# Optimization experiments

Hardware: AMD Instinct MI355X
Metric: run time of the kernel (lower is better)

The kernel has to match this reference:

```python
import jax, jax.numpy as jnp
import numpy as np

BSZ, SEQ, D, NHEAD, NLAYER, DFF, NQ = 4, 48, 256, 2, 2, 2048, 512
LN_EPS = 1e-5
NEG = jnp.float32(-1e30)


def _layernorm(x, w, b):
    m = jnp.mean(x, axis=-1, keepdims=True)
    v = jnp.mean((x - m) ** 2, axis=-1, keepdims=True)
    return (x - m) / jnp.sqrt(v + LN_EPS) * w + b


def _span_max(x):
    # Cumulative span max: span[b,s,e] = max(x[b,s:e+1]) for e>=s, else 0.
    B, S, H = x.shape
    padded = jnp.concatenate([x, jnp.full((B, S, H), NEG, x.dtype)], axis=1)  # [B,2S,H]

    def step(tmp, i):
        shifted = jax.lax.dynamic_slice(padded, (0, i, 0), (B, S, H))  # x shifted left by i, padded with -inf
        tmp = jnp.maximum(tmp, shifted)  # tmp[b,s] = max(x[b,s:s+i+1])
        return tmp, tmp

    _, ys = jax.lax.scan(step, jnp.full((B, S, H), NEG, x.dtype), jnp.arange(S))
    # ys: [width, B, start, H]; span[b,s,e] = ys[e-s, b, s]
    si = jnp.arange(S)[:, None]
    ei = jnp.arange(S)[None, :]
    w = jnp.clip(ei - si, 0, S - 1)
    span = ys[w, :, jnp.broadcast_to(si, (S, S))]  # [S_start, S_end, B, H]
    span = jnp.where((ei >= si)[:, :, None, None], span, 0.0)
    return span.transpose(2, 0, 1, 3)  # [B,S,S,H]


def _mha(x, wi, bi, wo, bo, kpm):
    # x: [B,T,D]; kpm: [B,T] bool, True = masked key
    B, T, Dm = x.shape
    hd = Dm // NHEAD
    qkv = x @ wi.T + bi
    q, k, v = jnp.split(qkv, 3, axis=-1)
    rs = lambda a: a.reshape(B, T, NHEAD, hd).transpose(0, 2, 1, 3)
    q, k, v = rs(q), rs(k), rs(v)
    scores = jnp.einsum('bhqd,bhkd->bhqk', q, k) * (1.0 / np.sqrt(hd))
    scores = jnp.where(kpm[:, None, None, :], -1e9, scores)
    p = jax.nn.softmax(scores, axis=-1)
    o = jnp.einsum('bhqk,bhkd->bhqd', p, v).transpose(0, 2, 1, 3).reshape(B, T, Dm)
    return o @ wo.T + bo


def _encoder(x, kpm, iw, ib, ow, ob, l1w, l1b, l2w, l2b, f1w, f1b, f2w, f2b, fw, fb):
    # Post-norm torch TransformerEncoder (eval mode, relu, no dropout)
    for l in range(NLAYER):
        a = _mha(x, iw[l], ib[l], ow[l], ob[l], kpm)
        x = _layernorm(x + a, l1w[l], l1b[l])
        f = jax.nn.relu(x @ f1w[l].T + f1b[l]) @ f2w[l].T + f2b[l]
        x = _layernorm(x + f, l2w[l], l2b[l])
    return _layernorm(x, fw, fb)


def _forward(enc, iw, ib, ow, ob, l1w, l1b, l2w, l2b, f1w, f1b, f2w, f2b, fw, fb, s1, e1, qb, s2, e2):
    span = _span_max(enc)  # [B,S,S,D]
    idx = jnp.arange(SEQ)
    kpm2d = idx[None, :] < idx[:, None]  # [start,end]: True where end < start
    kpm = jnp.broadcast_to(kpm2d.reshape(1, SEQ * SEQ), (BSZ, SEQ * SEQ))
    out = _encoder(span.reshape(BSZ, SEQ * SEQ, D), kpm, iw, ib, ow, ob, l1w, l1b, l2w, l2b, f1w, f1b, f2w, f2b, fw, fb)
    out = out.reshape(BSZ, SEQ, SEQ, D)
    res1 = out[qb, s1, e1]
    res2 = out[qb, s2, e2]
    return res1, res2


def setup_inputs() -> dict:
    key = jax.random.key(0)
    ks = jax.random.split(key, 16)
    sc = 0.02
    enc = jax.random.normal(ks[0], (BSZ, SEQ, D), jnp.float32)
    inp = {
        'encoded_input': enc,
        'in_proj_w': jax.random.normal(ks[1], (NLAYER, 3 * D, D), jnp.float32) * sc,
        'in_proj_b': jnp.zeros((NLAYER, 3 * D), jnp.float32),
        'out_proj_w': jax.random.normal(ks[2], (NLAYER, D, D), jnp.float32) * sc,
        'out_proj_b': jnp.zeros((NLAYER, D), jnp.float32),
        'ln1_w': jnp.ones((NLAYER, D), jnp.float32),
        'ln1_b': jnp.zeros((NLAYER, D), jnp.float32),
        'ln2_w': jnp.ones((NLAYER, D), jnp.float32),
        'ln2_b': jnp.zeros((NLAYER, D), jnp.float32),
        'ff1_w': jax.random.normal(ks[3], (NLAYER, DFF, D), jnp.float32) * sc,
        'ff1_b': jnp.zeros((NLAYER, DFF), jnp.float32),
        'ff2_w': jax.random.normal(ks[4], (NLAYER, D, DFF), jnp.float32) * sc,
        'ff2_b': jnp.zeros((NLAYER, D), jnp.float32),
        'fln_w': jnp.ones((D,), jnp.float32),
        'fln_b': jnp.zeros((D,), jnp.float32),
    }
    s1 = jax.random.randint(ks[5], (NQ,), 0, SEQ)
    e1 = jnp.minimum(s1 + jax.random.randint(ks[6], (NQ,), 0, SEQ), SEQ - 1)
    s2 = jax.random.randint(ks[7], (NQ,), 0, SEQ)
    e2 = jnp.minimum(s2 + jax.random.randint(ks[8], (NQ,), 0, SEQ), SEQ - 1)
    inp['start_ids_1'] = s1
    inp['end_ids_1'] = e1
    inp['query_batch_idx'] = jax.random.randint(ks[9], (NQ,), 0, BSZ)
    inp['start_ids_2'] = s2
    inp['end_ids_2'] = e2
    return inp


def reference(encoded_input, in_proj_w, in_proj_b, out_proj_w, out_proj_b, ln1_w, ln1_b, ln2_w, ln2_b, ff1_w, ff1_b, ff2_w, ff2_b, fln_w, fln_b, start_ids_1, end_ids_1, query_batch_idx, start_ids_2, end_ids_2):
    return _forward(encoded_input, in_proj_w, in_proj_b, out_proj_w, out_proj_b, ln1_w, ln1_b, ln2_w, ln2_b, ff1_w, ff1_b, ff2_w, ff2_b, fln_w, fln_b, start_ids_1, end_ids_1, query_batch_idx, start_ids_2, end_ids_2)
```

## Files before the change

kernel.cpp:

```cpp
#include <hip/hip_runtime.h>
#include <hip/hip_bf16.h>

#define BSZ 4
#define SEQ 48
#define DMODEL 256
#define NHEAD 2
#define HD 128
#define NLAYERS 2
#define DFF_C 2048
#define NQ_C 512
#define NV 1176
#define NTOT (BSZ * NV)
#define NVP 1216
#define KSPLIT 5
#define SCALE 0.088388347648318447f

typedef unsigned short u16;
typedef __attribute__((ext_vector_type(8))) short bf16x8;
typedef __attribute__((ext_vector_type(4))) float f32x4;

__device__ inline u16 f2b(float f) {
    __hip_bfloat16 h = __float2bfloat16(f);
    return *reinterpret_cast<u16*>(&h);
}
__device__ inline void storeval(float* p, float v) { *p = v; }
__device__ inline void storeval(u16* p, float v) { *p = f2b(v); }

__global__ __launch_bounds__(256) void castspan_kernel(
    const float* __restrict__ iw, const float* __restrict__ ow,
    const float* __restrict__ f1w, const float* __restrict__ f2w,
    u16* __restrict__ iwb, u16* __restrict__ owb,
    u16* __restrict__ f1wb, u16* __restrict__ f2wb,
    const float* __restrict__ enc, float* __restrict__ X,
    u16* __restrict__ Xb) {
    int bid = blockIdx.x;
    if (bid < 2560) {
        int i = bid * 256 + threadIdx.x;
        const float* src;
        u16* dst;
        int off;
        if (i < 98304)       { src = iw;  dst = iwb;  off = i; }
        else if (i < 131072) { src = ow;  dst = owb;  off = i - 98304; }
        else if (i < 393216) { src = f1w; dst = f1wb; off = i - 131072; }
        else                 { src = f2w; dst = f2wb; off = i - 393216; }
        float4 v = *(const float4*)(src + (size_t)off * 4);
        *(ushort4*)(dst + (size_t)off * 4) =
            make_ushort4(f2b(v.x), f2b(v.y), f2b(v.z), f2b(v.w));
    } else {
        int sb = bid - 2560;
        int i = sb % SEQ, b = sb / SEQ, h = threadIdx.x;
        int tb = i * SEQ - (i * (i - 1)) / 2 - i;
        float run = -1e30f;
        for (int j = i; j < SEQ; ++j) {
            run = fmaxf(run, enc[((size_t)b * SEQ + j) * DMODEL + h]);
            size_t idx = ((size_t)b * NV + tb + j) * DMODEL + h;
            X[idx] = run;
            Xb[idx] = f2b(run);
        }
    }
}

template <typename OutT, bool RELU, bool ATOMIC, int BK>
__global__ __launch_bounds__(256) void mm_kernel(
    const u16* __restrict__ A, const u16* __restrict__ W,
    const float* __restrict__ bias, const float* __restrict__ Res,
    OutT* __restrict__ C, int N, int K, int lda, int ldw, int ldc,
    float alpha, int WV, int KC) {
    __shared__ u16 As[64][BK + 8];
    __shared__ u16 Ws[64][BK + 8];
    const float4 fz = make_float4(0.f, 0.f, 0.f, 0.f);
    int ks = blockIdx.z;
    int kb = ks * KC, ke = min(K, kb + KC);
    int p0 = blockIdx.x * 64, n0 = blockIdx.y * 64;
    int tid = threadIdx.x, lane = tid & 63, w = tid >> 6;
    int col_l = lane & 15, quad = lane >> 4;
    f32x4 acc[4] = {};
    for (int k0 = kb; k0 < ke; k0 += BK) {
        int r = tid >> 2, seg = (tid & 3) * (BK / 4);
        {
            int gn = n0 + r;
            const u16* ap = A + (size_t)gn * lda + k0 + seg;
#pragma unroll
            for (int j = 0; j < BK / 32; ++j) {
                float4 av = fz;
                if (gn < N) av = *(const float4*)(ap + j * 8);
                *(float4*)&As[r][seg + j * 8] = av;
            }
        }
        {
            int gp = p0 + r;
            const u16* wp = W + (size_t)gp * ldw + k0 + seg;
#pragma unroll
            for (int j = 0; j < BK / 32; ++j) {
                float4 wv = fz;
                if (gp < WV) wv = *(const float4*)(wp + j * 8);
                *(float4*)&Ws[r][seg + j * 8] = wv;
            }
        }
        __syncthreads();
        bf16x8 a[BK / 32];
#pragma unroll
        for (int kf = 0; kf < BK / 32; ++kf)
            a[kf] = *(const bf16x8*)&As[w * 16 + col_l][kf * 32 + quad * 8];
#pragma unroll
        for (int c = 0; c < 4; ++c) {
#pragma unroll
            for (int kf = 0; kf < BK / 32; ++kf) {
                bf16x8 b = *(const bf16x8*)&Ws[c * 16 + col_l][kf * 32 + quad * 8];
                acc[c] = __builtin_amdgcn_mfma_f32_16x16x32_bf16(a[kf], b, acc[c], 0, 0, 0);
            }
        }
        __syncthreads();
    }
#pragma unroll
    for (int c = 0; c < 4; ++c) {
        int col = p0 + c * 16 + col_l;
        float bv = bias ? bias[col] : 0.f;
#pragma unroll
        for (int reg = 0; reg < 4; ++reg) {
            int row = n0 + w * 16 + quad * 4 + reg;
            if (row < N) {
                float v = acc[c][reg] * alpha + bv;
                if (Res) v += Res[(size_t)row * ldc + col];
                if (RELU) v = fmaxf(v, 0.f);
                if (ATOMIC) {
                    unsafeAtomicAdd((float*)&C[(size_t)row * ldc + col], v);
                } else {
                    storeval(&C[(size_t)row * ldc + col], v);
                }
            }
        }
    }
}

__global__ __launch_bounds__(256) void vtrans_kernel(const u16* __restrict__ QKVb,
                                                     u16* __restrict__ VT) {
    __shared__ u16 T[64][66];
    const float4 fz = make_float4(0.f, 0.f, 0.f, 0.f);
    int kt = blockIdx.x, dt = blockIdx.y, bh = blockIdx.z;
    int b = bh >> 1, h = bh & 1;
    size_t rb = (size_t)b * NV;
    int tid = threadIdx.x;
    {
        int r = tid >> 2, cs = (tid & 3) * 16;
        int key = kt * 64 + r;
        float4 v0 = fz, v1 = fz;
        if (key < NV) {
            const u16* vp = QKVb + (rb + key) * 768 + 2 * DMODEL + h * HD + dt * 64 + cs;
            v0 = *(const float4*)vp;
            v1 = *(const float4*)(vp + 8);
        }
        *(float4*)&T[r][cs] = v0;
        *(float4*)&T[r][cs + 8] = v1;
    }
    __syncthreads();
    {
        int dl = tid >> 2, ks2 = (tid & 3) * 16;
        u16 tmp[16];
#pragma unroll
        for (int j = 0; j < 16; ++j) tmp[j] = T[ks2 + j][dl];
        u16* dst = VT + ((size_t)bh * HD + dt * 64 + dl) * NVP + kt * 64 + ks2;
        *(float4*)dst = *(float4*)&tmp[0];
        *(float4*)(dst + 8) = *(float4*)&tmp[8];
    }
}

__global__ __launch_bounds__(256) void flash_kernel(const u16* __restrict__ QKVb,
                                                    const u16* __restrict__ VT,
                                                    float* __restrict__ Opart,
                                                    float* __restrict__ ML) {
    __shared__ u16 Ks[64][136];
    __shared__ u16 Vt[128][72];
    __shared__ u16 Ps[4][16][72];
    const float4 fz = make_float4(0.f, 0.f, 0.f, 0.f);
    int tid = threadIdx.x, lane = tid & 63, w = tid >> 6;
    int col_l = lane & 15, quad = lane >> 4;
    int bh = blockIdx.y, b = bh >> 1, h = bh & 1;
    int ks = blockIdx.z;
    int t0 = ks * 4, tcnt = min(4, 19 - t0);
    size_t rb = (size_t)b * NV;
    int q0 = blockIdx.x * 64, wq0 = q0 + w * 16;

    float4 qv[4];
    {
        int qrow = wq0 + col_l;
        if (qrow < NV) {
            const u16* qp = QKVb + (rb + qrow) * 768 + h * HD + quad * 8;
#pragma unroll
            for (int kf = 0; kf < 4; ++kf) qv[kf] = *(const float4*)(qp + kf * 32);
        } else {
#pragma unroll
            for (int kf = 0; kf < 4; ++kf) qv[kf] = fz;
        }
    }

    f32x4 oacc[8] = {};
    float m_run[4], l_run[4];
#pragma unroll
    for (int r = 0; r < 4; ++r) { m_run[r] = -1e30f; l_run[r] = 0.f; }

    for (int it = 0; it < tcnt; ++it) {
        int kt = (t0 + it) * 64;
        {
            int r = tid >> 2, seg = (tid & 3) * 32;
            int key = kt + r;
            const u16* kp = QKVb + (rb + key) * 768 + DMODEL + h * HD + seg;
#pragma unroll
            for (int t4 = 0; t4 < 4; ++t4) {
                float4 v = fz;
                if (key < NV) v = *(const float4*)(kp + t4 * 8);
                *(float4*)&Ks[r][seg + t4 * 8] = v;
            }
        }
        {
            int d = tid >> 1, half = (tid & 1) * 32;
            const u16* vp = VT + ((size_t)bh * HD + d) * NVP + kt + half;
#pragma unroll
            for (int t4 = 0; t4 < 4; ++t4)
                *(float4*)&Vt[d][half + t4 * 8] = *(const float4*)(vp + t4 * 8);
        }
        __syncthreads();

        f32x4 s[4] = {};
#pragma unroll
        for (int c = 0; c < 4; ++c)
#pragma unroll
            for (int kf = 0; kf < 4; ++kf) {
                bf16x8 kfr = *(const bf16x8*)&Ks[c * 16 + col_l][kf * 32 + quad * 8];
                s[c] = __builtin_amdgcn_mfma_f32_16x16x32_bf16(
                    *(const bf16x8*)&qv[kf], kfr, s[c], 0, 0, 0);
            }

        float pv[4][4];
#pragma unroll
        for (int c = 0; c < 4; ++c) {
            bool kvalid = (kt + c * 16 + col_l) < NV;
#pragma unroll
            for (int r = 0; r < 4; ++r)
                pv[c][r] = kvalid ? s[c][r] * SCALE : -1e30f;
        }
        float al[4];
#pragma unroll
        for (int r = 0; r < 4; ++r) {
            float mx = fmaxf(fmaxf(pv[0][r], pv[1][r]), fmaxf(pv[2][r], pv[3][r]));
#pragma unroll
            for (int off = 1; off < 16; off <<= 1)
                mx = fmaxf(mx, __shfl_xor(mx, off));
            float mn = fmaxf(m_run[r], mx);
            al[r] = __expf(m_run[r] - mn);
            m_run[r] = mn;
            float sum = 0.f;
#pragma unroll
            for (int c = 0; c < 4; ++c) {
                float p = __expf(pv[c][r] - mn);
                pv[c][r] = p;
                sum += p;
            }
#pragma unroll
            for (int off = 1; off < 16; off <<= 1) sum += __shfl_xor(sum, off);
            l_run[r] = l_run[r] * al[r] + sum;
        }
#pragma unroll
        for (int ct = 0; ct < 8; ++ct)
#pragma unroll
            for (int r = 0; r < 4; ++r) oacc[ct][r] *= al[r];

#pragma unroll
        for (int c = 0; c < 4; ++c)
#pragma unroll
            for (int r = 0; r < 4; ++r)
                Ps[w][quad * 4 + r][c * 16 + col_l] = f2b(pv[c][r]);
        bf16x8 pf0 = *(const bf16x8*)&Ps[w][col_l][quad * 8];
        bf16x8 pf1 = *(const bf16x8*)&Ps[w][col_l][32 + quad * 8];
#pragma unroll
        for (int ct = 0; ct < 8; ++ct) {
            bf16x8 v0 = *(const bf16x8*)&Vt[ct * 16 + col_l][quad * 8];
            bf16x8 v1 = *(const bf16x8*)&Vt[ct * 16 + col_l][32 + quad * 8];
            oacc[ct] = __builtin_amdgcn_mfma_f32_16x16x32_bf16(pf0, v0, oacc[ct], 0, 0, 0);
            oacc[ct] = __builtin_amdgcn_mfma_f32_16x16x32_bf16(pf1, v1, oacc[ct], 0, 0, 0);
        }
        __syncthreads();
    }

    size_t slab = (size_t)(ks * 8 + bh) * NVP;
#pragma unroll
    for (int ct = 0; ct < 8; ++ct)
#pragma unroll
        for (int r = 0; r < 4; ++r) {
            int row = wq0 + quad * 4 + r;
            Opart[(slab + row) * HD + ct * 16 + col_l] = oacc[ct][r];
        }
    if (col_l == 0) {
#pragma unroll
        for (int r = 0; r < 4; ++r) {
            int row = wq0 + quad * 4 + r;
            ML[(slab + row) * 2 + 0] = m_run[r];
            ML[(slab + row) * 2 + 1] = l_run[r];
        }
    }
}

__global__ __launch_bounds__(256) void comb_kernel(const float* __restrict__ Opart,
                                                   const float* __restrict__ ML,
                                                   u16* __restrict__ Obuf) {
    int bh = blockIdx.y, b = bh >> 1, h = bh & 1;
    int tid = threadIdx.x;
    int row = blockIdx.x * 2 + (tid >> 7);
    int d = tid & 127;
    if (row >= NV) return;
    float m[KSPLIT], l[KSPLIT];
#pragma unroll
    for (int i = 0; i < KSPLIT; ++i) {
        size_t mb = ((size_t)(i * 8 + bh) * NVP + row) * 2;
        m[i] = ML[mb];
        l[i] = ML[mb + 1];
    }
    float M = m[0];
#pragma unroll
    for (int i = 1; i < KSPLIT; ++i) M = fmaxf(M, m[i]);
    float wsum = 0.f, o = 0.f;
#pragma unroll
    for (int i = 0; i < KSPLIT; ++i) {
        float wi = __expf(m[i] - M);
        wsum += l[i] * wi;
        o += Opart[((size_t)(i * 8 + bh) * NVP + row) * HD + d] * wi;
    }
    Obuf[((size_t)b * NV + row) * DMODEL + h * HD + d] = f2b(o / wsum);
}

__global__ __launch_bounds__(256) void ln_kernel(const float* __restrict__ Xin,
                                                 const float* __restrict__ w,
                                                 const float* __restrict__ bb,
                                                 float* __restrict__ Y,
                                                 u16* __restrict__ Yb,
                                                 const float* __restrict__ fb2,
                                                 float* __restrict__ A2out) {
    int wv = threadIdx.x >> 6, lane = threadIdx.x & 63;
    int r = blockIdx.x * 4 + wv;
    size_t base = (size_t)r * DMODEL + lane * 4;
    float4 v = *(const float4*)(Xin + base);
    float s1 = v.x + v.y + v.z + v.w;
    float s2 = v.x * v.x + v.y * v.y + v.z * v.z + v.w * v.w;
#pragma unroll
    for (int off = 32; off > 0; off >>= 1) {
        s1 += __shfl_xor(s1, off);
        s2 += __shfl_xor(s2, off);
    }
    float mean = s1 * (1.f / DMODEL);
    float var = s2 * (1.f / DMODEL) - mean * mean;
    float rstd = rsqrtf(var + 1e-5f);
    float4 w4 = *(const float4*)(w + lane * 4);
    float4 b4 = *(const float4*)(bb + lane * 4);
    float o0 = (v.x - mean) * rstd * w4.x + b4.x;
    float o1 = (v.y - mean) * rstd * w4.y + b4.y;
    float o2 = (v.z - mean) * rstd * w4.z + b4.z;
    float o3 = (v.w - mean) * rstd * w4.w + b4.w;
    *(float4*)(Y + base) = make_float4(o0, o1, o2, o3);
    *(ushort4*)(Yb + base) = make_ushort4(f2b(o0), f2b(o1), f2b(o2), f2b(o3));
    if (A2out) {
        float4 f4 = *(const float4*)(fb2 + lane * 4);
        *(float4*)(A2out + base) = make_float4(o0 + f4.x, o1 + f4.y, o2 + f4.z, o3 + f4.w);
    }
}

__global__ __launch_bounds__(64) void gatherln_kernel(const float* __restrict__ X,
                                                      const float* __restrict__ fw,
                                                      const float* __restrict__ fb,
                                                      const int* __restrict__ s1,
                                                      const int* __restrict__ e1,
                                                      const int* __restrict__ qb,
                                                      const int* __restrict__ s2,
                                                      const int* __restrict__ e2,
                                                      float* __restrict__ out) {
    int q = blockIdx.x, which = blockIdx.y, lane = threadIdx.x;
    int s = which ? s2[q] : s1[q];
    int e = which ? e2[q] : e1[q];
    int b = qb[q];
    int t = s * SEQ - (s * (s - 1)) / 2 + (e - s);
    if (t < 0) t = 0;
    if (t >= NV) t = NV - 1;
    size_t base = ((size_t)b * NV + t) * DMODEL + lane * 4;
    float4 v = *(const float4*)(X + base);
    float s1v = v.x + v.y + v.z + v.w;
    float s2v = v.x * v.x + v.y * v.y + v.z * v.z + v.w * v.w;
#pragma unroll
    for (int off = 32; off > 0; off >>= 1) {
        s1v += __shfl_xor(s1v, off);
        s2v += __shfl_xor(s2v, off);
    }
    float mean = s1v * (1.f / DMODEL);
    float var = s2v * (1.f / DMODEL) - mean * mean;
    float rstd = rsqrtf(var + 1e-5f);
    float4 w4 = *(const float4*)(fw + lane * 4);
    float4 b4 = *(const float4*)(fb + lane * 4);
    float o0 = (v.x - mean) * rstd * w4.x + b4.x;
    float o1 = (v.y - mean) * rstd * w4.y + b4.y;
    float o2 = (v.z - mean) * rstd * w4.z + b4.z;
    float o3 = (v.w - mean) * rstd * w4.w + b4.w;
    *(float4*)(out + ((size_t)which * NQ_C + q) * DMODEL + lane * 4) =
        make_float4(o0, o1, o2, o3);
}

extern "C" void kernel_launch(void* const* d_in, const int* in_sizes, int n_in,
                              void* d_out, int out_size, void* d_ws, size_t ws_size,
                              hipStream_t stream) {
    const float* enc = (const float*)d_in[0];
    const float* iw  = (const float*)d_in[1];
    const float* ib  = (const float*)d_in[2];
    const float* ow  = (const float*)d_in[3];
    const float* ob  = (const float*)d_in[4];
    const float* l1w = (const float*)d_in[5];
    const float* l1b = (const float*)d_in[6];
    const float* l2w = (const float*)d_in[7];
    const float* l2b = (const float*)d_in[8];
    const float* f1w = (const float*)d_in[9];
    const float* f1b = (const float*)d_in[10];
    const float* f2w = (const float*)d_in[11];
    const float* f2b_ = (const float*)d_in[12];
    const float* flw = (const float*)d_in[13];
    const float* flb = (const float*)d_in[14];
    const int* s1 = (const int*)d_in[15];
    const int* e1 = (const int*)d_in[16];
    const int* qb = (const int*)d_in[17];
    const int* s2 = (const int*)d_in[18];
    const int* e2 = (const int*)d_in[19];
    float* out = (float*)d_out;

    char* p = (char*)d_ws;
    float* X     = (float*)p;  p += (size_t)NTOT * DMODEL * 4;
    float* A2    = (float*)p;  p += (size_t)NTOT * DMODEL * 4;
    u16* Xb      = (u16*)p;    p += (size_t)NTOT * DMODEL * 2;
    u16* Obuf    = (u16*)p;    p += (size_t)NTOT * DMODEL * 2;
    u16* QKVb    = (u16*)p;    p += (size_t)NTOT * 3 * DMODEL * 2;
    u16* VT      = (u16*)p;    p += (size_t)8 * HD * NVP * 2;
    float* ML    = (float*)p;  p += (size_t)KSPLIT * 8 * NVP * 2 * 4;
    float* Opart = (float*)p;  p += (size_t)KSPLIT * 8 * NVP * HD * 4;
    u16* wb      = (u16*)p;
    u16* F1b     = (u16*)Opart;

    u16* iwb  = wb;
    u16* owb  = iwb + 2 * 3 * DMODEL * DMODEL;
    u16* f1wb = owb + 2 * DMODEL * DMODEL;
    u16* f2wb = f1wb + 2 * DFF_C * DMODEL;

    castspan_kernel<<<dim3(2752), 256, 0, stream>>>(iw, ow, f1w, f2w,
                                                    iwb, owb, f1wb, f2wb,
                                                    enc, X, Xb);

    for (int l = 0; l < NLAYERS; ++l) {
        mm_kernel<u16, false, false, 64><<<dim3(12, 74, 1), 256, 0, stream>>>(
            Xb, iwb + (size_t)l * 3 * DMODEL * DMODEL, ib + (size_t)l * 3 * DMODEL,
            nullptr, QKVb, NTOT, DMODEL, DMODEL, DMODEL, 3 * DMODEL, 1.f,
            3 * DMODEL, DMODEL);
        vtrans_kernel<<<dim3(19, 2, 8), 256, 0, stream>>>(QKVb, VT);
        flash_kernel<<<dim3(19, 8, KSPLIT), 256, 0, stream>>>(QKVb, VT, Opart, ML);
        comb_kernel<<<dim3(588, 8), 256, 0, stream>>>(Opart, ML, Obuf);
        mm_kernel<float, false, false, 64><<<dim3(4, 74, 1), 256, 0, stream>>>(
            Obuf, owb + (size_t)l * DMODEL * DMODEL, ob + (size_t)l * DMODEL,
            X, A2, NTOT, DMODEL, DMODEL, DMODEL, DMODEL, 1.f, DMODEL, DMODEL);
        ln_kernel<<<dim3(NTOT / 4), 256, 0, stream>>>(
            A2, l1w + (size_t)l * DMODEL, l1b + (size_t)l * DMODEL,
            X, Xb, f2b_ + (size_t)l * DMODEL, A2);
        mm_kernel<u16, true, false, 64><<<dim3(32, 74, 1), 256, 0, stream>>>(
            Xb, f1wb + (size_t)l * DFF_C * DMODEL, f1b + (size_t)l * DFF_C,
            nullptr, F1b, NTOT, DMODEL, DMODEL, DMODEL, DFF_C, 1.f, DFF_C, DMODEL);
        mm_kernel<float, false, true, 128><<<dim3(4, 74, 4), 256, 0, stream>>>(
            F1b, f2wb + (size_t)l * DMODEL * DFF_C, nullptr, nullptr, A2,
            NTOT, DFF_C, DFF_C, DFF_C, DMODEL, 1.f, DMODEL, 512);
        ln_kernel<<<dim3(NTOT / 4), 256, 0, stream>>>(
            A2, l2w + (size_t)l * DMODEL, l2b + (size_t)l * DMODEL,
            X, Xb, nullptr, nullptr);
    }
    gatherln_kernel<<<dim3(NQ_C, 2), 64, 0, stream>>>(X, flw, flb,
                                                      s1, e1, qb, s2, e2, out);
}
```

Baseline: 352.8 us.

## Replace atomic split-K with slab partials reduced in LayerNorm; widen FFN GEMM tiles

```diff
diff --git a/kernel.cpp b/kernel.cpp
--- a/kernel.cpp
+++ b/kernel.cpp
@@ -13,6 +13,8 @@
 #define NTOT (BSZ * NV)
 #define NVP 1216
 #define KSPLIT 5
+#define FSPLIT 4
+#define OSPLIT 2
 #define SCALE 0.088388347648318447f
 
 typedef unsigned short u16;
@@ -60,55 +62,49 @@
     }
 }
 
-template <typename OutT, bool RELU, bool ATOMIC, int BK>
+template <typename OutT, bool RELU>
 __global__ __launch_bounds__(256) void mm_kernel(
     const u16* __restrict__ A, const u16* __restrict__ W,
     const float* __restrict__ bias, const float* __restrict__ Res,
     OutT* __restrict__ C, int N, int K, int lda, int ldw, int ldc,
-    float alpha, int WV, int KC) {
-    __shared__ u16 As[64][BK + 8];
-    __shared__ u16 Ws[64][BK + 8];
+    float alpha, int WV, int KC, int splitRows) {
+    __shared__ u16 As[64][72];
+    __shared__ u16 Ws[64][72];
     const float4 fz = make_float4(0.f, 0.f, 0.f, 0.f);
     int ks = blockIdx.z;
     int kb = ks * KC, ke = min(K, kb + KC);
+    if (splitRows) C += (size_t)ks * splitRows * ldc;
     int p0 = blockIdx.x * 64, n0 = blockIdx.y * 64;
     int tid = threadIdx.x, lane = tid & 63, w = tid >> 6;
     int col_l = lane & 15, quad = lane >> 4;
     f32x4 acc[4] = {};
-    for (int k0 = kb; k0 < ke; k0 += BK) {
-        int r = tid >> 2, seg = (tid & 3) * (BK / 4);
+    for (int k0 = kb; k0 < ke; k0 += 64) {
+        int r = tid >> 2, seg = (tid & 3) * 16;
         {
             int gn = n0 + r;
             const u16* ap = A + (size_t)gn * lda + k0 + seg;
-#pragma unroll
-            for (int j = 0; j < BK / 32; ++j) {
-                float4 av = fz;
-                if (gn < N) av = *(const float4*)(ap + j * 8);
-                *(float4*)&As[r][seg + j * 8] = av;
-            }
+            float4 a0 = fz, a1 = fz;
+            if (gn < N) { a0 = *(const float4*)ap; a1 = *(const float4*)(ap + 8); }
+            *(float4*)&As[r][seg] = a0;
+            *(float4*)&As[r][seg + 8] = a1;
         }
         {
             int gp = p0 + r;
             const u16* wp = W + (size_t)gp * ldw + k0 + seg;
-#pragma unroll
-            for (int j = 0; j < BK / 32; ++j) {
-                float4 wv = fz;
-                if (gp < WV) wv = *(const float4*)(wp + j * 8);
-                *(float4*)&Ws[r][seg + j * 8] = wv;
-            }
+            float4 w0 = fz, w1 = fz;
+            if (gp < WV) { w0 = *(const float4*)wp; w1 = *(const float4*)(wp + 8); }
+            *(float4*)&Ws[r][seg] = w0;
+            *(float4*)&Ws[r][seg + 8] = w1;
         }
         __syncthreads();
-        bf16x8 a[BK / 32];
-#pragma unroll
-        for (int kf = 0; kf < BK / 32; ++kf)
-            a[kf] = *(const bf16x8*)&As[w * 16 + col_l][kf * 32 + quad * 8];
+        bf16x8 a0 = *(const bf16x8*)&As[w * 16 + col_l][quad * 8];
+        bf16x8 a1 = *(const bf16x8*)&As[w * 16 + col_l][32 + quad * 8];
 #pragma unroll
         for (int c = 0; c < 4; ++c) {
-#pragma unroll
-            for (int kf = 0; kf < BK / 32; ++kf) {
-                bf16x8 b = *(const bf16x8*)&Ws[c * 16 + col_l][kf * 32 + quad * 8];
-                acc[c] = __builtin_amdgcn_mfma_f32_16x16x32_bf16(a[kf], b, acc[c], 0, 0, 0);
-            }
+            bf16x8 b0 = *(const bf16x8*)&Ws[c * 16 + col_l][quad * 8];
+            bf16x8 b1 = *(const bf16x8*)&Ws[c * 16 + col_l][32 + quad * 8];
+            acc[c] = __builtin_amdgcn_mfma_f32_16x16x32_bf16(a0, b0, acc[c], 0, 0, 0);
+            acc[c] = __builtin_amdgcn_mfma_f32_16x16x32_bf16(a1, b1, acc[c], 0, 0, 0);
         }
         __syncthreads();
     }
@@ -123,11 +119,72 @@
                 float v = acc[c][reg] * alpha + bv;
                 if (Res) v += Res[(size_t)row * ldc + col];
                 if (RELU) v = fmaxf(v, 0.f);
-                if (ATOMIC) {
-                    unsafeAtomicAdd((float*)&C[(size_t)row * ldc + col], v);
-                } else {
-                    storeval(&C[(size_t)row * ldc + col], v);
-                }
+                storeval(&C[(size_t)row * ldc + col], v);
+            }
+        }
+    }
+}
+
+template <typename OutT, bool RELU>
+__global__ __launch_bounds__(256) void mmw_kernel(
+    const u16* __restrict__ A, const u16* __restrict__ W,
+    const float* __restrict__ bias,
+    OutT* __restrict__ C, int N, int K, int lda, int ldw, int ldc,
+    int WV, int KC, int splitRows) {
+    __shared__ u16 As[64][72];
+    __shared__ u16 Ws[128][72];
+    const float4 fz = make_float4(0.f, 0.f, 0.f, 0.f);
+    int ks = blockIdx.z;
+    int kb = ks * KC, ke = min(K, kb + KC);
+    if (splitRows) C += (size_t)ks * splitRows * ldc;
+    int p0 = blockIdx.x * 128, n0 = blockIdx.y * 64;
+    int tid = threadIdx.x, lane = tid & 63, w = tid >> 6;
+    int col_l = lane & 15, quad = lane >> 4;
+    f32x4 acc[8] = {};
+    for (int k0 = kb; k0 < ke; k0 += 64) {
+        {
+            int r = tid >> 2, seg = (tid & 3) * 16;
+            int gn = n0 + r;
+            const u16* ap = A + (size_t)gn * lda + k0 + seg;
+            float4 a0 = fz, a1 = fz;
+            if (gn < N) { a0 = *(const float4*)ap; a1 = *(const float4*)(ap + 8); }
+            *(float4*)&As[r][seg] = a0;
+            *(float4*)&As[r][seg + 8] = a1;
+        }
+        {
+            int r2 = tid >> 1, seg2 = (tid & 1) * 32;
+            int gp = p0 + r2;
+            const u16* wp = W + (size_t)gp * ldw + k0 + seg2;
+#pragma unroll
+            for (int j = 0; j < 4; ++j) {
+                float4 wv = fz;
+                if (gp < WV) wv = *(const float4*)(wp + j * 8);
+                *(float4*)&Ws[r2][seg2 + j * 8] = wv;
+            }
+        }
+        __syncthreads();
+        bf16x8 a0 = *(const bf16x8*)&As[w * 16 + col_l][quad * 8];
+        bf16x8 a1 = *(const bf16x8*)&As[w * 16 + col_l][32 + quad * 8];
+#pragma unroll
+        for (int c = 0; c < 8; ++c) {
+            bf16x8 b0 = *(const bf16x8*)&Ws[c * 16 + col_l][quad * 8];
+            bf16x8 b1 = *(const bf16x8*)&Ws[c * 16 + col_l][32 + quad * 8];
+            acc[c] = __builtin_amdgcn_mfma_f32_16x16x32_bf16(a0, b0, acc[c], 0, 0, 0);
+            acc[c] = __builtin_amdgcn_mfma_f32_16x16x32_bf16(a1, b1, acc[c], 0, 0, 0);
+        }
+        __syncthreads();
+    }
+#pragma unroll
+    for (int c = 0; c < 8; ++c) {
+        int col = p0 + c * 16 + col_l;
+        float bv = bias ? bias[col] : 0.f;
+#pragma unroll
+        for (int reg = 0; reg < 4; ++reg) {
+            int row = n0 + w * 16 + quad * 4 + reg;
+            if (row < N) {
+                float v = acc[c][reg] + bv;
+                if (RELU) v = fmaxf(v, 0.f);
+                storeval(&C[(size_t)row * ldc + col], v);
             }
         }
     }
@@ -328,17 +385,25 @@
     Obuf[((size_t)b * NV + row) * DMODEL + h * HD + d] = f2b(o / wsum);
 }
 
-__global__ __launch_bounds__(256) void ln_kernel(const float* __restrict__ Xin,
-                                                 const float* __restrict__ w,
-                                                 const float* __restrict__ bb,
-                                                 float* __restrict__ Y,
-                                                 u16* __restrict__ Yb,
-                                                 const float* __restrict__ fb2,
-                                                 float* __restrict__ A2out) {
+template <int NSLAB>
+__global__ __launch_bounds__(256) void redln_kernel(const float* __restrict__ Xres,
+                                                    const float* __restrict__ P,
+                                                    const float* __restrict__ cbias,
+                                                    const float* __restrict__ w,
+                                                    const float* __restrict__ bb,
+                                                    float* __restrict__ Y,
+                                                    u16* __restrict__ Yb) {
     int wv = threadIdx.x >> 6, lane = threadIdx.x & 63;
     int r = blockIdx.x * 4 + wv;
     size_t base = (size_t)r * DMODEL + lane * 4;
-    float4 v = *(const float4*)(Xin + base);
+    float4 v = *(const float4*)(Xres + base);
+    float4 c4 = *(const float4*)(cbias + lane * 4);
+    v.x += c4.x; v.y += c4.y; v.z += c4.z; v.w += c4.w;
+#pragma unroll
+    for (int z = 0; z < NSLAB; ++z) {
+        float4 p4 = *(const float4*)(P + (size_t)z * NTOT * DMODEL + base);
+        v.x += p4.x; v.y += p4.y; v.z += p4.z; v.w += p4.w;
+    }
     float s1 = v.x + v.y + v.z + v.w;
     float s2 = v.x * v.x + v.y * v.y + v.z * v.z + v.w * v.w;
 #pragma unroll
@@ -357,10 +422,6 @@
     float o3 = (v.w - mean) * rstd * w4.w + b4.w;
     *(float4*)(Y + base) = make_float4(o0, o1, o2, o3);
     *(ushort4*)(Yb + base) = make_ushort4(f2b(o0), f2b(o1), f2b(o2), f2b(o3));
-    if (A2out) {
-        float4 f4 = *(const float4*)(fb2 + lane * 4);
-        *(float4*)(A2out + base) = make_float4(o0 + f4.x, o1 + f4.y, o2 + f4.z, o3 + f4.w);
-    }
 }
 
 __global__ __launch_bounds__(64) void gatherln_kernel(const float* __restrict__ X,
@@ -428,13 +489,13 @@
 
     char* p = (char*)d_ws;
     float* X     = (float*)p;  p += (size_t)NTOT * DMODEL * 4;
-    float* A2    = (float*)p;  p += (size_t)NTOT * DMODEL * 4;
     u16* Xb      = (u16*)p;    p += (size_t)NTOT * DMODEL * 2;
     u16* Obuf    = (u16*)p;    p += (size_t)NTOT * DMODEL * 2;
     u16* QKVb    = (u16*)p;    p += (size_t)NTOT * 3 * DMODEL * 2;
     u16* VT      = (u16*)p;    p += (size_t)8 * HD * NVP * 2;
     float* ML    = (float*)p;  p += (size_t)KSPLIT * 8 * NVP * 2 * 4;
     float* Opart = (float*)p;  p += (size_t)KSPLIT * 8 * NVP * HD * 4;
+    float* Pbuf  = (float*)p;  p += (size_t)FSPLIT * NTOT * DMODEL * 4;
     u16* wb      = (u16*)p;
     u16* F1b     = (u16*)Opart;
 
@@ -448,28 +509,29 @@
                                                     enc, X, Xb);
 
     for (int l = 0; l < NLAYERS; ++l) {
-        mm_kernel<u16, false, false, 64><<<dim3(12, 74, 1), 256, 0, stream>>>(
+        mm_kernel<u16, false><<<dim3(12, 74, 1), 256, 0, stream>>>(
             Xb, iwb + (size_t)l * 3 * DMODEL * DMODEL, ib + (size_t)l * 3 * DMODEL,
             nullptr, QKVb, NTOT, DMODEL, DMODEL, DMODEL, 3 * DMODEL, 1.f,
-            3 * DMODEL, DMODEL);
+            3 * DMODEL, DMODEL, 0);
         vtrans_kernel<<<dim3(19, 2, 8), 256, 0, stream>>>(QKVb, VT);
         flash_kernel<<<dim3(19, 8, KSPLIT), 256, 0, stream>>>(QKVb, VT, Opart, ML);
         comb_kernel<<<dim3(588, 8), 256, 0, stream>>>(Opart, ML, Obuf);
-        mm_kernel<float, false, false, 64><<<dim3(4, 74, 1), 256, 0, stream>>>(
-            Obuf, owb + (size_t)l * DMODEL * DMODEL, ob + (size_t)l * DMODEL,
-            X, A2, NTOT, DMODEL, DMODEL, DMODEL, DMODEL, 1.f, DMODEL, DMODEL);
-        ln_kernel<<<dim3(NTOT / 4), 256, 0, stream>>>(
-            A2, l1w + (size_t)l * DMODEL, l1b + (size_t)l * DMODEL,
-            X, Xb, f2b_ + (size_t)l * DMODEL, A2);
-        mm_kernel<u16, true, false, 64><<<dim3(32, 74, 1), 256, 0, stream>>>(
+        mm_kernel<float, false><<<dim3(4, 74, OSPLIT), 256, 0, stream>>>(
+            Obuf, owb + (size_t)l * DMODEL * DMODEL, nullptr, nullptr, Pbuf,
+            NTOT, DMODEL, DMODEL, DMODEL, DMODEL, 1.f, DMODEL,
+            DMODEL / OSPLIT, NTOT);
+        redln_kernel<OSPLIT><<<dim3(NTOT / 4), 256, 0, stream>>>(
+            X, Pbuf, ob + (size_t)l * DMODEL,
+            l1w + (size_t)l * DMODEL, l1b + (size_t)l * DMODEL, X, Xb);
+        mmw_kernel<u16, true><<<dim3(16, 74, 1), 256, 0, stream>>>(
             Xb, f1wb + (size_t)l * DFF_C * DMODEL, f1b + (size_t)l * DFF_C,
-            nullptr, F1b, NTOT, DMODEL, DMODEL, DMODEL, DFF_C, 1.f, DFF_C, DMODEL);
-        mm_kernel<float, false, true, 128><<<dim3(4, 74, 4), 256, 0, stream>>>(
-            F1b, f2wb + (size_t)l * DMODEL * DFF_C, nullptr, nullptr, A2,
-            NTOT, DFF_C, DFF_C, DFF_C, DMODEL, 1.f, DMODEL, 512);
-        ln_kernel<<<dim3(NTOT / 4), 256, 0, stream>>>(
-            A2, l2w + (size_t)l * DMODEL, l2b + (size_t)l * DMODEL,
-            X, Xb, nullptr, nullptr);
+            F1b, NTOT, DMODEL, DMODEL, DMODEL, DFF_C, DFF_C, DMODEL, 0);
+        mmw_kernel<float, false><<<dim3(2, 74, FSPLIT), 256, 0, stream>>>(
+            F1b, f2wb + (size_t)l * DMODEL * DFF_C, nullptr, Pbuf,
+            NTOT, DFF_C, DFF_C, DFF_C, DMODEL, DMODEL, DFF_C / FSPLIT, NTOT);
+        redln_kernel<FSPLIT><<<dim3(NTOT / 4), 256, 0, stream>>>(
+            X, Pbuf, f2b_ + (size_t)l * DMODEL,
+            l2w + (size_t)l * DMODEL, l2b + (size_t)l * DMODEL, X, Xb);
     }
     gatherln_kernel<<<dim3(NQ_C, 2), 64, 0, stream>>>(X, flw, flb,
                                                       s1, e1, qb, s2, e2, out);
```

New measurement: 316.7 us. 10.2% less time.
